# Kernel tuning notes

Hardware: AMD Instinct MI355X
Metric: run time of the kernel (lower is better)

## Reference

```python
import jax, jax.numpy as jnp
import numpy as np

MAX_SEQ_LEN = 1000

def _ln(x, g, b, eps=1e-5):
    m = jnp.mean(x, -1, keepdims=True)
    v = jnp.var(x, -1, keepdims=True)
    return (x - m) * jax.lax.rsqrt(v + eps) * g + b

def _conv1d(x, k, b):
    # x [B,T,Cin], k [K,Cin,Cout], 'SAME' padding (odd kernel)
    return jax.lax.conv_general_dilated(x, k, (1,), 'SAME', dimension_numbers=('NWC', 'WIO', 'NWC')) + b

def _dwconv(x, w):
    # lightweight conv: softmax-normalized depthwise kernel, w [C,K]
    k = jnp.transpose(jax.nn.softmax(w, axis=1))[:, None, :]  # [K,1,C]
    return jax.lax.conv_general_dilated(x, k, (1,), 'SAME', dimension_numbers=('NWC', 'WIO', 'NWC'), feature_group_count=x.shape[-1])

def _conv2d(x, k, b):
    # x [B,H,W,Cin], k [kh,kw,Cin,Cout]
    return jax.lax.conv_general_dilated(x, k, (1, 1), 'SAME', dimension_numbers=('NHWC', 'HWIO', 'NHWC')) + b

def _lconv(x, mask, ln_g, ln_b, glu_w, glu_b, dw, out_w, out_b):
    # LConvBlock: LN -> GLU projection -> depthwise lightweight conv -> out proj -> residual, masked
    res = x
    h = _ln(x, ln_g, ln_b)
    h = h @ glu_w + glu_b
    a, g = jnp.split(h, 2, axis=-1)
    h = a * jax.nn.sigmoid(g)
    h = jnp.where(mask[..., None], 0.0, h)
    h = _dwconv(h, dw)
    h = h @ out_w + out_b
    h = h + res
    return jnp.where(mask[..., None], 0.0, h)

def _forward(content_embedding, speaker_embedding_B, rhythm_B, scaled_duration_outputs,
             in_w, in_b,
             lc0_ln_g, lc0_ln_b, lc0_glu_w, lc0_glu_b, lc0_dw, lc0_out_w, lc0_out_b,
             lc1_ln_g, lc1_ln_b, lc1_glu_w, lc1_glu_b, lc1_dw, lc1_out_w, lc1_out_b,
             p1_w, p1_b, p2_k, p2_b,
             cw_k, cw_b, cw_ln_g, cw_ln_b,
             mkb1_k, mkb1_b, mkb2_k, mkb2_b,
             lw_w, lw_b, ln_g, ln_b, text_mask):
    B, S, _ = content_embedding.shape
    spk = jnp.broadcast_to(speaker_embedding_B[:, None, :], (B, S, speaker_embedding_B.shape[-1]))
    x = jnp.concatenate([content_embedding, spk], -1) @ in_w + in_b
    # duration predictor
    V = _lconv(x, text_mask, lc0_ln_g, lc0_ln_b, lc0_glu_w, lc0_glu_b, lc0_dw, lc0_out_w, lc0_out_b)
    V = _lconv(V, text_mask, lc1_ln_g, lc1_ln_b, lc1_glu_w, lc1_glu_b, lc1_dw, lc1_out_w, lc1_out_b)
    D = jax.nn.softplus(V @ p1_w + p1_b)[..., 0]
    D = jnp.where(text_mask, 0.0, D)
    T = _conv1d(V, p2_k, p2_b)  # [B,S,upsampled_dim]
    # learnable upsampling
    pred_phoneme_len = scaled_duration_outputs.sum(-1)
    alpha_B = jax.lax.stop_gradient(pred_phoneme_len / rhythm_B) / D.sum(-1)
    sD = alpha_B[:, None] * D
    sV = alpha_B[:, None, None] * V
    sT = alpha_B[:, None, None] * T
    mel_len = jnp.clip(jnp.round(sD.sum(-1)).astype(jnp.int32), 1, MAX_SEQ_LEN)
    mel_mask = jnp.arange(MAX_SEQ_LEN)[None, :] >= mel_len[:, None]  # True = pad
    attn_mask = mel_mask[:, :, None] & text_mask[:, None, :]  # bmm(mel_mask, src_mask^T).bool()
    e_k = jnp.cumsum(sD, axis=1)
    s_k = e_k - sD
    t = jnp.arange(1, MAX_SEQ_LEN + 1, dtype=sD.dtype)[None, :, None]
    Sm = jnp.where(attn_mask, 0.0, t - s_k[:, None, :])
    Em = jnp.where(attn_mask, 0.0, e_k[:, None, :] - t)
    # conv_w block: conv1d -> relu -> LN
    Cv = _ln(jax.nn.relu(_conv1d(sV, cw_k, cw_b)), cw_ln_g, cw_ln_b)  # [B,S,CW]
    feat = jnp.concatenate([Sm[..., None], Em[..., None],
                            jnp.broadcast_to(Cv[:, None, :, :], (B, MAX_SEQ_LEN, S, Cv.shape[-1]))], -1)
    h = jax.nn.silu(_conv2d(feat, mkb1_k, mkb1_b))
    h = jax.nn.silu(_conv2d(h, mkb2_k, mkb2_b))
    Wsc = (h @ lw_w + lw_b)[..., 0]  # [B,mel,S]
    Wsc = jnp.where(attn_mask | text_mask[:, None, :], -jnp.inf, Wsc)
    Wmat = jax.nn.softmax(Wsc, axis=2)
    up = jnp.matmul(Wmat, sT)
    up = _ln(up, ln_g, ln_b)
    up = jnp.where(mel_mask[..., None], 0.0, up)
    return up, Wmat, alpha_B, mel_len, mel_mask

def setup_inputs() -> dict:
    key = jax.random.key(0)
    ks = iter(jax.random.split(key, 64))
    B, S, DC, DS, H, CW, MKB, K = 8, 256, 192, 64, 256, 16, 16, 3
    def w(shape, scale=0.02):
        return jax.random.normal(next(ks), shape, jnp.float32) * scale
    inp = {}
    inp['content_embedding'] = jax.random.normal(next(ks), (B, S, DC), jnp.float32)
    inp['speaker_embedding_B'] = jax.random.normal(next(ks), (B, DS), jnp.float32)
    inp['rhythm_B'] = 0.15 + 0.1 * jax.random.uniform(next(ks), (B,), jnp.float32)
    inp['scaled_duration_outputs'] = jax.random.uniform(next(ks), (B, S), jnp.float32)
    lens = jax.random.randint(next(ks), (B,), 200, S + 1)
    inp['text_mask'] = jnp.arange(S)[None, :] >= lens[:, None]
    inp['in_w'] = w((DC + DS, H)); inp['in_b'] = jnp.zeros((H,), jnp.float32)
    for i in range(2):
        inp[f'lc{i}_ln_g'] = jnp.ones((H,), jnp.float32); inp[f'lc{i}_ln_b'] = jnp.zeros((H,), jnp.float32)
        inp[f'lc{i}_glu_w'] = w((H, 2 * H)); inp[f'lc{i}_glu_b'] = jnp.zeros((2 * H,), jnp.float32)
        inp[f'lc{i}_dw'] = w((H, K), 1.0)
        inp[f'lc{i}_out_w'] = w((H, H)); inp[f'lc{i}_out_b'] = jnp.zeros((H,), jnp.float32)
    inp['p1_w'] = w((H, 1)); inp['p1_b'] = jnp.zeros((1,), jnp.float32)
    inp['p2_k'] = w((K, H, H)); inp['p2_b'] = jnp.zeros((H,), jnp.float32)
    inp['cw_k'] = w((K, H, CW)); inp['cw_b'] = jnp.zeros((CW,), jnp.float32)
    inp['cw_ln_g'] = jnp.ones((CW,), jnp.float32); inp['cw_ln_b'] = jnp.zeros((CW,), jnp.float32)
    inp['mkb1_k'] = w((K, K, CW + 2, MKB)); inp['mkb1_b'] = jnp.zeros((MKB,), jnp.float32)
    inp['mkb2_k'] = w((K, K, MKB, MKB)); inp['mkb2_b'] = jnp.zeros((MKB,), jnp.float32)
    inp['lw_w'] = w((MKB, 1)); inp['lw_b'] = jnp.zeros((1,), jnp.float32)
    inp['ln_g'] = jnp.ones((H,), jnp.float32); inp['ln_b'] = jnp.zeros((H,), jnp.float32)
    return inp

def reference(content_embedding, speaker_embedding_B, rhythm_B, scaled_duration_outputs,
              text_mask,
              in_w, in_b,
              lc0_ln_g, lc0_ln_b, lc0_glu_w, lc0_glu_b, lc0_dw, lc0_out_w, lc0_out_b,
              lc1_ln_g, lc1_ln_b, lc1_glu_w, lc1_glu_b, lc1_dw, lc1_out_w, lc1_out_b,
              p1_w, p1_b, p2_k, p2_b,
              cw_k, cw_b, cw_ln_g, cw_ln_b,
              mkb1_k, mkb1_b, mkb2_k, mkb2_b,
              lw_w, lw_b, ln_g, ln_b):
    return _forward(content_embedding, speaker_embedding_B, rhythm_B, scaled_duration_outputs,
                    in_w, in_b,
                    lc0_ln_g, lc0_ln_b, lc0_glu_w, lc0_glu_b, lc0_dw, lc0_out_w, lc0_out_b,
                    lc1_ln_g, lc1_ln_b, lc1_glu_w, lc1_glu_b, lc1_dw, lc1_out_w, lc1_out_b,
                    p1_w, p1_b, p2_k, p2_b,
                    cw_k, cw_b, cw_ln_g, cw_ln_b,
                    mkb1_k, mkb1_b, mkb2_k, mkb2_b,
                    lw_w, lw_b, ln_g, ln_b, text_mask)
```

## Files before the change

kernel.cpp:

```cpp
#include <hip/hip_runtime.h>
#include <math.h>

#define SS 256
#define HH 256
#define MLEN 1000
#define CWW 16
#define NOC 16
#define RB 24

typedef __attribute__((ext_vector_type(8))) short bfrag;
typedef __attribute__((ext_vector_type(4))) float ffrag;

#define WS_V2     1048576u
#define WS_STT    1835008u
#define WS_WB     2097152u
#define WS_CCV    2424832u
#define WS_SSV    2457600u
#define WS_CCI    2490368u
#define WS_SSI    2523136u
#define WS_CP     2555904u
#define WS_CV     2654208u
#define WS_EK     2686976u
#define WS_SK     2689024u
#define WS_ALPHA  2691072u
#define WS_MELI   2691080u
#define WS_TMASK  2691088u

#define PK_IN     0u
#define PK_GLU0   65536u
#define PK_GLU1   196608u
#define PK_OUT0   327680u
#define PK_OUT1   393216u
#define PK_P2     458752u

#define OUT_UP    0u
#define OUT_W     2048000u
#define OUT_ALPHA 4096000u
#define OUT_MLEN  4096008u
#define OUT_MMASK 4096016u

__device__ __forceinline__ unsigned bf16rne(float x){
  unsigned u=__float_as_uint(x);
  u += 0x7fffu + ((u>>16)&1u);
  return u;
}
__device__ __forceinline__ unsigned short bf16h(float x){ return (unsigned short)(bf16rne(x)>>16); }
__device__ __forceinline__ float bf2f(unsigned short u){ return __uint_as_float(((unsigned)u)<<16); }
__device__ __forceinline__ unsigned frag_idx(int k,int n,int KT){
  return (unsigned)(((((n>>4)*KT+(k>>5))*64 + ((k>>3)&3)*16 + (n&15))<<3) + (k&7));
}

__global__ __launch_bounds__(256) void k_prepmask(const void* __restrict__ traw,
    const float* __restrict__ in_w,
    const float* __restrict__ g0, const float* __restrict__ g1,
    const float* __restrict__ o0, const float* __restrict__ o1,
    const float* __restrict__ p2k, float* __restrict__ ws){
  int tid=threadIdx.x;
  if(blockIdx.x==256){
    __shared__ int s_fu, s_ff, s_nz;
    const unsigned char* mb=(const unsigned char*)traw;
    const unsigned int*  mw=(const unsigned int*)traw;
    if(tid==0){s_fu=0;s_ff=0;s_nz=0;}
    __syncthreads();
    int fu=0,ff=0,nz=0;
    for(int w=tid;w<512;w+=256){
      unsigned int v=mw[w];
      if(v){ nz=1; if(v==0x3F800000u) ff=1; else if(v&0xFFFFFF00u) fu=1; }
    }
    if(fu) atomicOr(&s_fu,1);
    if(ff) atomicOr(&s_ff,1);
    if(nz) atomicOr(&s_nz,1);
    __syncthreads();
    int words = (s_ff || (!s_fu && s_nz));
    for(int i=tid;i<2048;i+=256){
      unsigned int v = words ? mw[i] : (unsigned int)mb[i];
      ws[WS_TMASK+i] = v ? 1.0f : 0.0f;
    }
    return;
  }
  unsigned short* wb=(unsigned short*)(ws+WS_WB);
  int gid=blockIdx.x*256+tid, stride=65536;
  for(int i=gid;i<65536;i+=stride){ int k=i>>8,n=i&255; wb[PK_IN  +frag_idx(k,n,8)]=bf16h(in_w[i]); }
  for(int i=gid;i<131072;i+=stride){ int k=i>>9,n=i&511; wb[PK_GLU0+frag_idx(k,n,8)]=bf16h(g0[i]); }
  for(int i=gid;i<131072;i+=stride){ int k=i>>9,n=i&511; wb[PK_GLU1+frag_idx(k,n,8)]=bf16h(g1[i]); }
  for(int i=gid;i<65536;i+=stride){ int k=i>>8,n=i&255; wb[PK_OUT0+frag_idx(k,n,8)]=bf16h(o0[i]); }
  for(int i=gid;i<65536;i+=stride){ int k=i>>8,n=i&255; wb[PK_OUT1+frag_idx(k,n,8)]=bf16h(o1[i]); }
  for(int i=gid;i<196608;i+=stride){ int k3=i>>16,r=i&65535,k=r>>8,n=r&255;
    wb[PK_P2+(unsigned)k3*65536u+frag_idx(k,n,8)]=bf16h(p2k[i]); }
}

__global__ __launch_bounds__(256) void k_front(
    const float* __restrict__ ce, const float* __restrict__ spk,
    const unsigned short* __restrict__ wb, const float* __restrict__ in_b,
    const float* __restrict__ g0b, const float* __restrict__ ln0g, const float* __restrict__ ln0b,
    const float* __restrict__ dw0, const float* __restrict__ o0b,
    const float* __restrict__ g1b, const float* __restrict__ ln1g, const float* __restrict__ ln1b,
    const float* __restrict__ dw1, const float* __restrict__ o1b,
    const float* __restrict__ tmask, float* __restrict__ V2){
  __shared__ unsigned short Abf[16][264];
  __shared__ unsigned short Hb[16][264];
// ... 20 lines not shown
    tmL[tid]=(sI>=0&&sI<256)? tmask[b*256+sI] : 1.0f;
  }
  for(int it=0;it<16;it++){
    float v=0.f;
    int sI=s0-2+it;
    if(it<12 && sI>=0 && sI<256){
      int m=b*256+sI;
      v=(tid<192)? ce[m*192+tid] : spk[b*64+tid-192];
    }
    Abf[it][tid]=bf16h(v);
  }
  __syncthreads();
  {
    ffrag acc[4];
    #pragma unroll
    for(int j=0;j<4;j++){acc[j][0]=0;acc[j][1]=0;acc[j][2]=0;acc[j][3]=0;}
    #pragma unroll
    for(int kt=0;kt<8;kt++){
      bfrag af=*(const bfrag*)&Abf[lm][kt*32+lq*8];
      #pragma unroll
      for(int j=0;j<4;j++){
        int nt=w*4+j;
        bfrag bf=*(const bfrag*)(wb+PK_IN+((((unsigned)(nt*8+kt))*64u+(unsigned)lane)<<3));
        acc[j]=__builtin_amdgcn_mfma_f32_16x16x32_bf16(af,bf,acc[j],0,0,0);
      }
    }
    #pragma unroll
    for(int j=0;j<4;j++){
      int n=w*64+j*16+lm;
      float bn=in_b[n];
      #pragma unroll
      for(int reg=0;reg<4;reg++) Xf[lq*4+reg][n]=acc[j][reg]+bn;
    }
  }
  __syncthreads();
  {
    int r=tid>>4, seg=tid&15;
    if(r<12){
      float s=0.f,q=0.f;
      #pragma unroll
      for(int j4=0;j4<4;j4++){
        float4 v=*(const float4*)&Xf[r][seg*16+j4*4];
        s+=v.x+v.y+v.z+v.w; q+=v.x*v.x+v.y*v.y+v.z*v.z+v.w*v.w;
      }
      s+=__shfl_xor(s,1); q+=__shfl_xor(q,1);
      s+=__shfl_xor(s,2); q+=__shfl_xor(q,2);
      s+=__shfl_xor(s,4); q+=__shfl_xor(q,4);
      s+=__shfl_xor(s,8); q+=__shfl_xor(q,8);
      float mean=s*(1.0f/256.0f), rstd=rsqrtf(q*(1.0f/256.0f)-mean*mean+1e-5f);
      #pragma unroll
      for(int j4=0;j4<4;j4++){
        int c=seg*16+j4*4;
        float4 v=*(const float4*)&Xf[r][c];
        unsigned short q0=bf16h((v.x-mean)*rstd*ln0g[c+0]+ln0b[c+0]);
        unsigned short q1=bf16h((v.y-mean)*rstd*ln0g[c+1]+ln0b[c+1]);
        unsigned short q2=bf16h((v.z-mean)*rstd*ln0g[c+2]+ln0b[c+2]);
        unsigned short q3=bf16h((v.w-mean)*rstd*ln0g[c+3]+ln0b[c+3]);
        *(uint2*)&Abf[r][c]=make_uint2((unsigned)q0|((unsigned)q1<<16),(unsigned)q2|((unsigned)q3<<16));
      }
    } else {
      #pragma unroll
      for(int j4=0;j4<4;j4++) *(uint2*)&Abf[r][seg*16+j4*4]=make_uint2(0,0);
    }
  }
  __syncthreads();
  {
    ffrag aa[4],ag[4];
    #pragma unroll
    for(int j=0;j<4;j++){aa[j][0]=0;aa[j][1]=0;aa[j][2]=0;aa[j][3]=0;
                         ag[j][0]=0;ag[j][1]=0;ag[j][2]=0;ag[j][3]=0;}
    #pragma unroll
    for(int kt=0;kt<8;kt++){
      bfrag af=*(const bfrag*)&Abf[lm][kt*32+lq*8];
      #pragma unroll
      for(int j=0;j<4;j++){
        int nta=w*4+j, ntg=nta+16;
        bfrag bfa=*(const bfrag*)(wb+PK_GLU0+((((unsigned)(nta*8+kt))*64u+(unsigned)lane)<<3));
        bfrag bfg=*(const bfrag*)(wb+PK_GLU0+((((unsigned)(ntg*8+kt))*64u+(unsigned)lane)<<3));
        aa[j]=__builtin_amdgcn_mfma_f32_16x16x32_bf16(af,bfa,aa[j],0,0,0);
        ag[j]=__builtin_amdgcn_mfma_f32_16x16x32_bf16(af,bfg,ag[j],0,0,0);
      }
    }
    __syncthreads();
    #pragma unroll
    for(int j=0;j<4;j++){
      int n=w*64+j*16+lm;
      float ba=g0b[n], bg=g0b[n+256];
      #pragma unroll
      for(int reg=0;reg<4;reg++){
        int row=lq*4+reg;
        float a=aa[j][reg]+ba, g=ag[j][reg]+bg;
        float hv=a*(1.0f/(1.0f+__expf(-g)));
        if(row>=12||tmL[row]!=0.0f) hv=0.0f;
        Hb[row][n]=bf16h(hv);
      }
    }
  }
  __syncthreads();
  {
    float w0=dws[0][0][tid],w1=dws[0][1][tid],w2=dws[0][2][tid];
    for(int r=0;r<10;r++){
      float a=w0*bf2f(Hb[r][tid])+w1*bf2f(Hb[r+1][tid])+w2*bf2f(Hb[r+2][tid]);
      Abf[r][tid]=bf16h(a);
    }
    for(int r=10;r<16;r++) Abf[r][tid]=0;
  }
  __syncthreads();
  {
    ffrag acc[4];
    #pragma unroll
    for(int j=0;j<4;j++){acc[j][0]=0;acc[j][1]=0;acc[j][2]=0;acc[j][3]=0;}
    #pragma unroll
    for(int kt=0;kt<8;kt++){
      bfrag af=*(const bfrag*)&Abf[lm][kt*32+lq*8];
      #pragma unroll
      for(int j=0;j<4;j++){
        int nt=w*4+j;
        bfrag bf=*(const bfrag*)(wb+PK_OUT0+((((unsigned)(nt*8+kt))*64u+(unsigned)lane)<<3));
        acc[j]=__builtin_amdgcn_mfma_f32_16x16x32_bf16(af,bf,acc[j],0,0,0);
      }
    }
    #pragma unroll
    for(int j=0;j<4;j++){
      int n=w*64+j*16+lm;
      float bn=o0b[n];
      #pragma unroll
      for(int reg=0;reg<4;reg++){
        int row=lq*4+reg;
        float v=(row<10 && tmL[row+1]==0.0f)? acc[j][reg]+bn+Xf[row+1][n] : 0.0f;
        Vf[row][n]=v;
      }
    }
  }
  __syncthreads();
  {
    int r=tid>>4, seg=tid&15;
    if(r<10){
      float s=0.f,q=0.f;
      #pragma unroll
      for(int j4=0;j4<4;j4++){
        float4 v=*(const float4*)&Vf[r][seg*16+j4*4];
        s+=v.x+v.y+v.z+v.w; q+=v.x*v.x+v.y*v.y+v.z*v.z+v.w*v.w;
      }
      s+=__shfl_xor(s,1); q+=__shfl_xor(q,1);
      s+=__shfl_xor(s,2); q+=__shfl_xor(q,2);
      s+=__shfl_xor(s,4); q+=__shfl_xor(q,4);
      s+=__shfl_xor(s,8); q+=__shfl_xor(q,8);
      float mean=s*(1.0f/256.0f), rstd=rsqrtf(q*(1.0f/256.0f)-mean*mean+1e-5f);
      #pragma unroll
      for(int j4=0;j4<4;j4++){
        int c=seg*16+j4*4;
        float4 v=*(const float4*)&Vf[r][c];
        unsigned short q0=bf16h((v.x-mean)*rstd*ln1g[c+0]+ln1b[c+0]);
        unsigned short q1=bf16h((v.y-mean)*rstd*ln1g[c+1]+ln1b[c+1]);
        unsigned short q2=bf16h((v.z-mean)*rstd*ln1g[c+2]+ln1b[c+2]);
        unsigned short q3=bf16h((v.w-mean)*rstd*ln1g[c+3]+ln1b[c+3]);
        *(uint2*)&Abf[r][c]=make_uint2((unsigned)q0|((unsigned)q1<<16),(unsigned)q2|((unsigned)q3<<16));
      }
    } else {
      #pragma unroll
      for(int j4=0;j4<4;j4++) *(uint2*)&Abf[r][seg*16+j4*4]=make_uint2(0,0);
    }
  }
  __syncthreads();
  {
    ffrag aa[4],ag[4];
    #pragma unroll
    for(int j=0;j<4;j++){aa[j][0]=0;aa[j][1]=0;aa[j][2]=0;aa[j][3]=0;
                         ag[j][0]=0;ag[j][1]=0;ag[j][2]=0;ag[j][3]=0;}
    #pragma unroll
    for(int kt=0;kt<8;kt++){
      bfrag af=*(const bfrag*)&Abf[lm][kt*32+lq*8];
      #pragma unroll
      for(int j=0;j<4;j++){
        int nta=w*4+j, ntg=nta+16;
        bfrag bfa=*(const bfrag*)(wb+PK_GLU1+((((unsigned)(nta*8+kt))*64u+(unsigned)lane)<<3));
        bfrag bfg=*(const bfrag*)(wb+PK_GLU1+((((unsigned)(ntg*8+kt))*64u+(unsigned)lane)<<3));
        aa[j]=__builtin_amdgcn_mfma_f32_16x16x32_bf16(af,bfa,aa[j],0,0,0);
        ag[j]=__builtin_amdgcn_mfma_f32_16x16x32_bf16(af,bfg,ag[j],0,0,0);
      }
    }
    __syncthreads();
    #pragma unroll
    for(int j=0;j<4;j++){
      int n=w*64+j*16+lm;
      float ba=g1b[n], bg=g1b[n+256];
      #pragma unroll
      for(int reg=0;reg<4;reg++){
        int row=lq*4+reg;
        float a=aa[j][reg]+ba, g=ag[j][reg]+bg;
        float hv=a*(1.0f/(1.0f+__expf(-g)));
        if(row>=10||tmL[row+1]!=0.0f) hv=0.0f;
        Hb[row][n]=bf16h(hv);
      }
    }
  }
  __syncthreads();
  {
    float w0=dws[1][0][tid],w1=dws[1][1][tid],w2=dws[1][2][tid];
    for(int r=0;r<8;r++){
      float a=w0*bf2f(Hb[r][tid])+w1*bf2f(Hb[r+1][tid])+w2*bf2f(Hb[r+2][tid]);
      Abf[r][tid]=bf16h(a);
    }
    for(int r=8;r<16;r++) Abf[r][tid]=0;
  }
  __syncthreads();
  {
    ffrag acc[4];
    #pragma unroll
    for(int j=0;j<4;j++){acc[j][0]=0;acc[j][1]=0;acc[j][2]=0;acc[j][3]=0;}
    #pragma unroll
    for(int kt=0;kt<8;kt++){
      bfrag af=*(const bfrag*)&Abf[lm][kt*32+lq*8];
      #pragma unroll
      for(int j=0;j<4;j++){
        int nt=w*4+j;
        bfrag bf=*(const bfrag*)(wb+PK_OUT1+((((unsigned)(nt*8+kt))*64u+(unsigned)lane)<<3));
        acc[j]=__builtin_amdgcn_mfma_f32_16x16x32_bf16(af,bf,acc[j],0,0,0);
      }
    }
    #pragma unroll
    for(int j=0;j<4;j++){
      int n=w*64+j*16+lm;
      float bn=o1b[n];
      #pragma unroll
      for(int reg=0;reg<4;reg++){
        int row=lq*4+reg;
        if(row<8){
          float v=(tmL[row+2]!=0.0f)? 0.0f : acc[j][reg]+bn+Vf[row+1][n];
          V2[(unsigned)(b*256+s0+row)*256u+n]=v;
        }
      }
    }
  }
}

__global__ __launch_bounds__(256) void k_dur(const float* __restrict__ V2, const float* __restrict__ p1w,
    const float* __restrict__ p1b, const float* __restrict__ sdo, const float* __restrict__ rhythm,
    float* __restrict__ ws, float* __restrict__ outp){
  __shared__ float p1[HH];
  __shared__ float sd[SS];
  __shared__ float red[16];
  int b=blockIdx.x, tid=threadIdx.x;
  int wid=tid>>6, lane=tid&63;
// ... 146 lines not shown
    #pragma unroll
    for(int oc=0;oc<NOC;oc++){ float bb2=mkb1b[oc]; ccv[oc]=bb2; cci[oc]=bb2; ssv[oc]=0.f; ssi[oc]=0.f; }
    for(int dt=0;dt<3;dt++){
      float acc[NOC];
      #pragma unroll
      for(int oc=0;oc<NOC;oc++) acc[oc]=0.f;
      #pragma unroll
      for(int ds=0;ds<3;ds++){
        #pragma unroll
        for(int ic=0;ic<CWW;ic++){
          float v=CvL[tid+ds][ic];
          #pragma unroll
          for(int oc=0;oc<NOC;oc++) acc[oc]+=v*k1c[dt][ds][ic][oc];
        }
      }
      for(int oc=0;oc<NOC;oc++) cpg[(unsigned)(dt*SS+tid)*NOC+oc]=acc[oc];
      float va[16],vb[16],ia[16],ib2[16];
      #pragma unroll
      for(int oc=0;oc<NOC;oc++){ va[oc]=0.f; vb[oc]=0.f; ia[oc]=0.f; ib2[oc]=0.f; }
      #pragma unroll
      for(int ds=0;ds<3;ds++){
        int j=tid+ds;
        float inb=(j>=1&&j<=SS)?1.0f:0.0f;
        float fb=fiE[j];
        float skv=skE[j], ekv=ekE[j];
        #pragma unroll
        for(int oc=0;oc<NOC;oc++){
          float ka=kab[dt][ds][0][oc], kb=kab[dt][ds][1][oc];
          float d=ka-kb, e=kb*ekv-ka*skv;
          va[oc]+=inb*d; vb[oc]+=inb*e; ia[oc]+=fb*d; ib2[oc]+=fb*e;
        }
      }
      float dtf=(float)dt;
      #pragma unroll
      for(int oc=0;oc<NOC;oc++){
        ccv[oc]+=acc[oc]+vb[oc]+dtf*va[oc]; ssv[oc]+=va[oc];
        cci[oc]+=acc[oc]+ib2[oc]+dtf*ia[oc]; ssi[oc]+=ia[oc];
      }
    }
    unsigned base=(unsigned)(b*SS+tid)*16u;
    for(int oc=0;oc<NOC;oc++){
      ws[WS_CCV+base+oc]=ccv[oc];
      ws[WS_SSV+base+oc]=ssv[oc];
      ws[WS_CCI+base+oc]=cci[oc];
      ws[WS_SSI+base+oc]=ssi[oc];
    }
  }
}

__global__ __launch_bounds__(256,4) void k_stageB(
    const float* __restrict__ ws, const float* __restrict__ mkb1k, const float* __restrict__ mkb1b,
    const float* __restrict__ mkb2k, const float* __restrict__ mkb2b,
    const float* __restrict__ lww, const float* __restrict__ lwb,
    float* __restrict__ outp){
  __shared__ short ringh[3][258][RB];
  __shared__ float skL[258], ekL[258];
  __shared__ unsigned char finC[260];
  __shared__ __align__(16) float wscL[SS];
  __shared__ float red[16];
  int bx=blockIdx.x, b=bx/125, chunk=bx%125, t0=chunk*8, tid=threadIdx.x;
  int wid=tid>>6, lane=tid&63;
  int lq=lane>>4, lm=lane&15;
  if(tid<258){
    float sk=0.f, ek=0.f; unsigned char fin=0;
    if(tid>=1 && tid<=SS){
      sk=ws[WS_SK+b*SS+tid-1];
      ek=ws[WS_EK+b*SS+tid-1];
      fin=(ws[WS_TMASK+b*SS+tid-1]!=0.0f)?0:1;
    }
    skL[tid]=sk; ekL[tid]=ek; finC[tid]=fin;
  }
  if(tid<72){
    int sl=tid/24, rem=tid%24;
    int row=(rem<12)?0:257, c=(rem%12)*2;
    *(int*)&ringh[sl][row][c]=0;
  }
  int mel=((const int*)ws)[WS_MELI+b];
  __syncthreads();

  const float* cpb=ws+WS_CP+(unsigned)b*3*SS*NOC;

  unsigned offA[5]; int dtL[5], zgL[5];
  bfrag bfw[5];
  {
    #pragma unroll
    for(int i=0;i<5;i++){
      int g=4*i+lq;
      int dt,ds,hf,zg;
      if(g<18){ dt=g/6; int rm=g-6*dt; ds=rm>>1; hf=rm&1; zg=0; }
      else { dt=0; ds=0; hf=0; zg=1; }
      int srow=wid*64+lm+ds;
      offA[i]=(unsigned)((srow*RB+8*hf)*2);
      dtL[i]=dt; zgL[i]=zg;
      int pk[4];
      if(!zg){
        #pragma unroll
        for(int j=0;j<4;j++){
          unsigned u0=bf16rne(mkb2k[(8*g+2*j)*NOC+lm]);
          unsigned u1=bf16rne(mkb2k[(8*g+2*j+1)*NOC+lm]);
          pk[j]=(int)((u0>>16)|(u1&0xffff0000u));
        }
      } else pk[0]=pk[1]=pk[2]=pk[3]=0;
      bfw[i]=__builtin_bit_cast(bfrag, make_int4(pk[0],pk[1],pk[2],pk[3]));
    }
  }
  float b2v=mkb2b[lm];
  float lwwv=lww[lm];
  float lwb0=lwb[0];
  const char* ringB=(const char*)&ringh[0][0][0];
  bfrag azero={};

  auto conv1row=[&](int T){
    int s=tid;
    float acc[NOC];
    bool fv=(T>=1)&&(T<=998)&&(T+1<mel);
    bool fi=(T>=2)&&(T<=998)&&(T-1>=mel);
    if(fv||fi){
      const float* cc=ws+(fv?WS_CCV:WS_CCI)+(unsigned)(b*SS+s)*16u;
      const float* s2=ws+(fv?WS_SSV:WS_SSI)+(unsigned)(b*SS+s)*16u;
      float Tf=(float)T;
      #pragma unroll
      for(int q=0;q<4;q++){
        float4 c4=((const float4*)cc)[q];
        float4 s4=((const float4*)s2)[q];
        acc[4*q+0]=c4.x+Tf*s4.x; acc[4*q+1]=c4.y+Tf*s4.y;
        acc[4*q+2]=c4.z+Tf*s4.z; acc[4*q+3]=c4.w+Tf*s4.w;
      }
    } else {
      #pragma unroll
      for(int oc=0;oc<NOC;oc++) acc[oc]=mkb1b[oc];
      #pragma unroll
      for(int dt=0;dt<3;dt++){
        int tr=T+dt-1;
        if(tr<0||tr>=MLEN) continue;
        bool valid=(tr<mel);
        float tt=(float)(tr+1);
        float gg[3], hh[3];
        #pragma unroll
        for(int ds=0;ds<3;ds++){
          int j=s+ds;
          float f = valid ? ((j>=1&&j<=SS)?1.0f:0.0f) : (float)finC[j];
          gg[ds]=f*(tt-skL[j]);
          hh[ds]=f*(ekL[j]-tt);
        }
        const float* cpr=cpb+(unsigned)(dt*SS+s)*NOC;
        float4 c0=((const float4*)cpr)[0], c1=((const float4*)cpr)[1];
        float4 c2=((const float4*)cpr)[2], c3=((const float4*)cpr)[3];
        acc[0]+=c0.x; acc[1]+=c0.y; acc[2]+=c0.z; acc[3]+=c0.w;
        acc[4]+=c1.x; acc[5]+=c1.y; acc[6]+=c1.z; acc[7]+=c1.w;
        acc[8]+=c2.x; acc[9]+=c2.y; acc[10]+=c2.z; acc[11]+=c2.w;
        acc[12]+=c3.x; acc[13]+=c3.y; acc[14]+=c3.z; acc[15]+=c3.w;
        #pragma unroll
        for(int ds=0;ds<3;ds++){
          const float* kA=mkb1k+((dt*3+ds)*18+0)*NOC;
          const float* kB=mkb1k+((dt*3+ds)*18+1)*NOC;
          #pragma unroll
          for(int oc=0;oc<NOC;oc++) acc[oc]+=gg[ds]*kA[oc]+hh[ds]*kB[oc];
        }
      }
    }
    int slot=T%3;
    int pk[8];
    #pragma unroll
    for(int j=0;j<8;j++){
      float x0=acc[2*j], x1=acc[2*j+1];
      float s0=x0/(1.0f+__expf(-x0));
      float s1=x1/(1.0f+__expf(-x1));
      unsigned u0=bf16rne(s0), u1=bf16rne(s1);
      pk[j]=(int)((u0>>16)|(u1&0xffff0000u));
    }
    int4* dst=(int4*)&ringh[slot][s+1][0];
    dst[0]=make_int4(pk[0],pk[1],pk[2],pk[3]);
    dst[1]=make_int4(pk[4],pk[5],pk[6],pk[7]);
  };

  if(t0>0) conv1row(t0-1);
  conv1row(t0);

  #pragma unroll 1
  for(int r=0;r<8;r++){
    int t=t0+r;
    if(t+1<MLEN) conv1row(t+1);
    __syncthreads();
    int tmod=t%3;
    ffrag acc2[4];
    #pragma unroll
    for(int tt=0;tt<4;tt++){ acc2[tt][0]=b2v; acc2[tt][1]=b2v; acc2[tt][2]=b2v; acc2[tt][3]=b2v; }
    #pragma unroll
    for(int i=0;i<5;i++){
      int dt=dtL[i];
      int x=tmod+dt+2; x=(x>=3)?x-3:x; x=(x>=3)?x-3:x;
      int tr=t+dt-1;
      bool av=((unsigned)tr<(unsigned)MLEN)&&(!zgL[i]);
      const char* rp=ringB+(unsigned)x*(258u*RB*2u)+offA[i];
      #pragma unroll
      for(int tt=0;tt<4;tt++){
        int4 ra=*(const int4*)(rp+tt*(16*RB*2));
        bfrag a=av?__builtin_bit_cast(bfrag,ra):azero;
        acc2[tt]=__builtin_amdgcn_mfma_f32_16x16x32_bf16(a,bfw[i],acc2[tt],0,0,0);
      }
    }
    #pragma unroll
    for(int tt=0;tt<4;tt++){
      float out4[4];
      #pragma unroll
      for(int q=0;q<4;q++){
        float xx=acc2[tt][q];
        float pv=(xx/(1.0f+__expf(-xx)))*lwwv;
        pv+=__shfl_xor(pv,1); pv+=__shfl_xor(pv,2); pv+=__shfl_xor(pv,4); pv+=__shfl_xor(pv,8);
        out4[q]=pv+lwb0;
      }
      if(lm==0){
        *(float4*)&wscL[wid*64+tt*16+lq*4]=make_float4(out4[0],out4[1],out4[2],out4[3]);
      }
    }
    __syncthreads();
    float fm=(float)finC[tid+1];
    float wsc=wscL[tid];
    float val=(fm!=0.0f)?wsc:-3.0e38f;
    float mx=val;
    for(int off=32;off;off>>=1) mx=fmaxf(mx,__shfl_down(mx,off));
    if(lane==0) red[wid]=mx;
    __syncthreads();
    mx=fmaxf(fmaxf(red[0],red[1]),fmaxf(red[2],red[3]));
    float e=(fm!=0.0f)?__expf(wsc-mx):0.0f;
    float sm=e;
    for(int off=32;off;off>>=1) sm+=__shfl_down(sm,off);
    if(lane==0) red[8+wid]=sm;
    __syncthreads();
    sm=red[8]+red[9]+red[10]+red[11];
    outp[OUT_W+(unsigned)(b*MLEN+t)*SS+tid]=e/sm;
    __syncthreads();
  }
}

__global__ __launch_bounds__(256) void k_up(const float* __restrict__ ws,
    const float* __restrict__ lng, const float* __restrict__ lnb, float* __restrict__ outp){
  __shared__ unsigned short Wbf[16][264];
  __shared__ float UpL[16][264];
  __shared__ float gb[2][256];
  int bx=blockIdx.x, b=bx/63, tile=bx%63, t0=tile*16, tid=threadIdx.x;
  gb[0][tid]=lng[tid]; gb[1][tid]=lnb[tid];
  for(int it=0;it<16;it++){
    int t=t0+it;
    float v=(t<MLEN)? outp[OUT_W+(unsigned)(b*MLEN+t)*256u+tid] : 0.0f;
    Wbf[it][tid]=bf16h(v);
  }
  int mel=((const int*)ws)[WS_MELI+b];
  __syncthreads();
  int w=tid>>6, lane=tid&63, lq=lane>>4, lm=lane&15;
  const unsigned short* stt=(const unsigned short*)(ws+WS_STT)+(unsigned)b*65536u;
  ffrag acc[4];
  #pragma unroll
  for(int tt=0;tt<4;tt++){ acc[tt][0]=0;acc[tt][1]=0;acc[tt][2]=0;acc[tt][3]=0; }
  #pragma unroll
  for(int kt=0;kt<8;kt++){
    bfrag af=*(const bfrag*)&Wbf[lm][kt*32+lq*8];
    #pragma unroll
    for(int tt=0;tt<4;tt++){
      int n=w*64+tt*16+lm;
      bfrag bf=*(const bfrag*)(stt+((unsigned)n<<8)+(unsigned)(kt*32+lq*8));
      acc[tt]=__builtin_amdgcn_mfma_f32_16x16x32_bf16(af,bf,acc[tt],0,0,0);
    }
  }
  #pragma unroll
  for(int tt=0;tt<4;tt++){
    #pragma unroll
    for(int reg=0;reg<4;reg++)
      UpL[lq*4+reg][w*64+tt*16+lm]=acc[tt][reg];
  }
  __syncthreads();
  int r=tid>>4, seg=tid&15;
  float s=0.f,q=0.f;
  #pragma unroll
  for(int j4=0;j4<4;j4++){
    float4 v=*(const float4*)&UpL[r][seg*16+j4*4];
    s+=v.x+v.y+v.z+v.w; q+=v.x*v.x+v.y*v.y+v.z*v.z+v.w*v.w;
  }
  s+=__shfl_xor(s,1); q+=__shfl_xor(q,1);
  s+=__shfl_xor(s,2); q+=__shfl_xor(q,2);
  s+=__shfl_xor(s,4); q+=__shfl_xor(q,4);
  s+=__shfl_xor(s,8); q+=__shfl_xor(q,8);
  float mean=s*(1.0f/256.0f), rstd=rsqrtf(q*(1.0f/256.0f)-mean*mean+1e-5f);
  int t=t0+r;
  if(t<MLEN){
    bool vld=(t<mel);
    #pragma unroll
    for(int j4=0;j4<4;j4++){
      int c=seg*16+j4*4;
      float4 v=*(const float4*)&UpL[r][c];
      float4 o;
      o.x=vld?((v.x-mean)*rstd*gb[0][c+0]+gb[1][c+0]):0.0f;
      o.y=vld?((v.y-mean)*rstd*gb[0][c+1]+gb[1][c+1]):0.0f;
      o.z=vld?((v.z-mean)*rstd*gb[0][c+2]+gb[1][c+2]):0.0f;
      o.w=vld?((v.w-mean)*rstd*gb[0][c+3]+gb[1][c+3]):0.0f;
      *(float4*)&outp[OUT_UP+(unsigned)(b*MLEN+t)*256u+c]=o;
    }
  }
}

extern "C" void kernel_launch(void* const* d_in, const int* in_sizes, int n_in,
                              void* d_out, int out_size, void* d_ws, size_t ws_size,
                              hipStream_t stream){
  const float* ce   =(const float*)d_in[0];
  const float* spk  =(const float*)d_in[1];
  const float* rhy  =(const float*)d_in[2];
  const float* sdo  =(const float*)d_in[3];
  const void*  tmr  =d_in[4];
  const float* in_w =(const float*)d_in[5];
  const float* in_b =(const float*)d_in[6];
  const float* l0lg =(const float*)d_in[7];
  const float* l0lb =(const float*)d_in[8];
  const float* l0gw =(const float*)d_in[9];
  const float* l0gb =(const float*)d_in[10];
  const float* l0dw =(const float*)d_in[11];
  const float* l0ow =(const float*)d_in[12];
  const float* l0ob =(const float*)d_in[13];
  const float* l1lg =(const float*)d_in[14];
  const float* l1lb =(const float*)d_in[15];
  const float* l1gw =(const float*)d_in[16];
  const float* l1gb =(const float*)d_in[17];
  const float* l1dw =(const float*)d_in[18];
  const float* l1ow =(const float*)d_in[19];
  const float* l1ob =(const float*)d_in[20];
  const float* p1w  =(const float*)d_in[21];
  const float* p1b  =(const float*)d_in[22];
  const float* p2k  =(const float*)d_in[23];
  const float* p2b  =(const float*)d_in[24];
  const float* cwk  =(const float*)d_in[25];
  const float* cwb  =(const float*)d_in[26];
  const float* cwg  =(const float*)d_in[27];
  const float* cwbe =(const float*)d_in[28];
  const float* m1k  =(const float*)d_in[29];
  const float* m1b  =(const float*)d_in[30];
  const float* m2k  =(const float*)d_in[31];
  const float* m2b  =(const float*)d_in[32];
  const float* lww  =(const float*)d_in[33];
  const float* lwbp =(const float*)d_in[34];
  const float* lng  =(const float*)d_in[35];
  const float* lnb  =(const float*)d_in[36];
  float* ws=(float*)d_ws;
  float* outp=(float*)d_out;
  const unsigned short* wbb=(const unsigned short*)(ws+WS_WB);

  k_prepmask<<<257,256,0,stream>>>(tmr, in_w, l0gw, l1gw, l0ow, l1ow, p2k, ws);
  k_front   <<<256,256,0,stream>>>(ce, spk, wbb, in_b,
                                   l0gb, l0lg, l0lb, l0dw, l0ob,
                                   l1gb, l1lg, l1lb, l1dw, l1ob,
                                   ws+WS_TMASK, ws+WS_V2);
  k_dur     <<<8,256,0,stream>>>(ws+WS_V2, p1w, p1b, sdo, rhy, ws, outp);
  k_post    <<<392,256,0,stream>>>(ws+WS_V2, wbb+PK_P2, p2b, cwk, cwb, cwg, cwbe, m1k, m1b, ws);
  k_stageB  <<<1000,256,0,stream>>>(ws, m1k, m1b, m2k, m2b, lww, lwbp, outp);
  k_up      <<<504,256,0,stream>>>(ws, lng, lnb, outp);
}
```

Measured before the change: 313.2 us.

## Fuse upsample LayerNorm kernel into stageB and swap MFMA operand roles

Removes the separate k_up kernel. Each stageB block now computes the W@STT upsample matmul and LayerNorm for its own 8 frames, reusing the ring LDS buffer. This drops one launch and the separate pass that reread the attention weights. The second conv's MFMA operands are swapped so each lane holds four output channels, which replaces the 16-lane shuffle reduction with a few xor-shuffles. Out-of-range rows are now zero-filled in the ring, so the per-fragment validity selects go away. In exchange, half of each 16-row MFMA tile is wasted on zero padding, since blocks only cover 8 frames.

```diff
diff --git a/kernel.cpp b/kernel.cpp
--- a/kernel.cpp
+++ b/kernel.cpp
@@ -562,8 +562,9 @@
     const float* __restrict__ ws, const float* __restrict__ mkb1k, const float* __restrict__ mkb1b,
     const float* __restrict__ mkb2k, const float* __restrict__ mkb2b,
     const float* __restrict__ lww, const float* __restrict__ lwb,
+    const float* __restrict__ lng, const float* __restrict__ lnb,
     float* __restrict__ outp){
-  __shared__ short ringh[3][258][RB];
+  __shared__ __align__(16) short ringh[3][258][RB];
   __shared__ float skL[258], ekL[258];
   __shared__ unsigned char finC[260];
   __shared__ __align__(16) float wscL[SS];
@@ -590,20 +591,20 @@
 
   const float* cpb=ws+WS_CP+(unsigned)b*3*SS*NOC;
 
-  unsigned offA[5]; int dtL[5], zgL[5];
+  unsigned offA[5]; int dtL[5];
   bfrag bfw[5];
   {
     #pragma unroll
     for(int i=0;i<5;i++){
       int g=4*i+lq;
-      int dt,ds,hf,zg;
-      if(g<18){ dt=g/6; int rm=g-6*dt; ds=rm>>1; hf=rm&1; zg=0; }
-      else { dt=0; ds=0; hf=0; zg=1; }
+      int dt,ds,hf;
+      if(g<18){ dt=g/6; int rm=g-6*dt; ds=rm>>1; hf=rm&1; }
+      else { dt=0; ds=0; hf=0; }
       int srow=wid*64+lm+ds;
       offA[i]=(unsigned)((srow*RB+8*hf)*2);
-      dtL[i]=dt; zgL[i]=zg;
+      dtL[i]=dt;
       int pk[4];
-      if(!zg){
+      if(g<18){
         #pragma unroll
         for(int j=0;j<4;j++){
           unsigned u0=bf16rne(mkb2k[(8*g+2*j)*NOC+lm]);
@@ -614,13 +615,19 @@
       bfw[i]=__builtin_bit_cast(bfrag, make_int4(pk[0],pk[1],pk[2],pk[3]));
     }
   }
-  float b2v=mkb2b[lm];
-  float lwwv=lww[lm];
+  float4 b2q=*(const float4*)&mkb2b[lq*4];
+  float4 lw4=*(const float4*)&lww[lq*4];
   float lwb0=lwb[0];
   const char* ringB=(const char*)&ringh[0][0][0];
-  bfrag azero={};
 
   auto conv1row=[&](int T){
+    int slot=((T%3)+3)%3;
+    int4* dst=(int4*)&ringh[slot][tid+1][0];
+    if((unsigned)T>=(unsigned)MLEN){
+      dst[0]=make_int4(0,0,0,0);
+      dst[1]=make_int4(0,0,0,0);
+      return;
+    }
     int s=tid;
     float acc[NOC];
     bool fv=(T>=1)&&(T<=998)&&(T+1<mel);
@@ -669,7 +676,6 @@
         }
       }
     }
-    int slot=T%3;
     int pk[8];
     #pragma unroll
     for(int j=0;j<8;j++){
@@ -679,50 +685,43 @@
       unsigned u0=bf16rne(s0), u1=bf16rne(s1);
       pk[j]=(int)((u0>>16)|(u1&0xffff0000u));
     }
-    int4* dst=(int4*)&ringh[slot][s+1][0];
     dst[0]=make_int4(pk[0],pk[1],pk[2],pk[3]);
     dst[1]=make_int4(pk[4],pk[5],pk[6],pk[7]);
   };
 
-  if(t0>0) conv1row(t0-1);
+  conv1row(t0-1);
   conv1row(t0);
 
   #pragma unroll 1
   for(int r=0;r<8;r++){
     int t=t0+r;
-    if(t+1<MLEN) conv1row(t+1);
+    conv1row(t+1);
     __syncthreads();
     int tmod=t%3;
     ffrag acc2[4];
     #pragma unroll
-    for(int tt=0;tt<4;tt++){ acc2[tt][0]=b2v; acc2[tt][1]=b2v; acc2[tt][2]=b2v; acc2[tt][3]=b2v; }
+    for(int tt=0;tt<4;tt++){ acc2[tt][0]=b2q.x; acc2[tt][1]=b2q.y; acc2[tt][2]=b2q.z; acc2[tt][3]=b2q.w; }
     #pragma unroll
     for(int i=0;i<5;i++){
       int dt=dtL[i];
       int x=tmod+dt+2; x=(x>=3)?x-3:x; x=(x>=3)?x-3:x;
-      int tr=t+dt-1;
-      bool av=((unsigned)tr<(unsigned)MLEN)&&(!zgL[i]);
       const char* rp=ringB+(unsigned)x*(258u*RB*2u)+offA[i];
       #pragma unroll
       for(int tt=0;tt<4;tt++){
-        int4 ra=*(const int4*)(rp+tt*(16*RB*2));
-        bfrag a=av?__builtin_bit_cast(bfrag,ra):azero;
-        acc2[tt]=__builtin_amdgcn_mfma_f32_16x16x32_bf16(a,bfw[i],acc2[tt],0,0,0);
+        bfrag a=*(const bfrag*)(rp+tt*(16*RB*2));
+        acc2[tt]=__builtin_amdgcn_mfma_f32_16x16x32_bf16(bfw[i],a,acc2[tt],0,0,0);
       }
     }
     #pragma unroll
     for(int tt=0;tt<4;tt++){
-      float out4[4];
-      #pragma unroll
-      for(int q=0;q<4;q++){
-        float xx=acc2[tt][q];
-        float pv=(xx/(1.0f+__expf(-xx)))*lwwv;
-        pv+=__shfl_xor(pv,1); pv+=__shfl_xor(pv,2); pv+=__shfl_xor(pv,4); pv+=__shfl_xor(pv,8);
-        out4[q]=pv+lwb0;
-      }
-      if(lm==0){
-        *(float4*)&wscL[wid*64+tt*16+lq*4]=make_float4(out4[0],out4[1],out4[2],out4[3]);
-      }
+      float x0=acc2[tt][0], x1=acc2[tt][1], x2=acc2[tt][2], x3=acc2[tt][3];
+      float pvs=(x0/(1.0f+__expf(-x0)))*lw4.x
+               +(x1/(1.0f+__expf(-x1)))*lw4.y
+               +(x2/(1.0f+__expf(-x2)))*lw4.z
+               +(x3/(1.0f+__expf(-x3)))*lw4.w;
+      pvs+=__shfl_xor(pvs,16);
+      pvs+=__shfl_xor(pvs,32);
+      if(lane<16) wscL[wid*64+tt*16+lane]=pvs+lwb0;
     }
     __syncthreads();
     float fm=(float)finC[tid+1];
@@ -739,72 +738,71 @@
     if(lane==0) red[8+wid]=sm;
     __syncthreads();
     sm=red[8]+red[9]+red[10]+red[11];
-    outp[OUT_W+(unsigned)(b*MLEN+t)*SS+tid]=e/sm;
-    __syncthreads();
-  }
-}
-
-__global__ __launch_bounds__(256) void k_up(const float* __restrict__ ws,
-    const float* __restrict__ lng, const float* __restrict__ lnb, float* __restrict__ outp){
-  __shared__ unsigned short Wbf[16][264];
-  __shared__ float UpL[16][264];
-  __shared__ float gb[2][256];
-  int bx=blockIdx.x, b=bx/63, tile=bx%63, t0=tile*16, tid=threadIdx.x;
-  gb[0][tid]=lng[tid]; gb[1][tid]=lnb[tid];
-  for(int it=0;it<16;it++){
-    int t=t0+it;
-    float v=(t<MLEN)? outp[OUT_W+(unsigned)(b*MLEN+t)*256u+tid] : 0.0f;
-    Wbf[it][tid]=bf16h(v);
-  }
-  int mel=((const int*)ws)[WS_MELI+b];
-  __syncthreads();
-  int w=tid>>6, lane=tid&63, lq=lane>>4, lm=lane&15;
+    float p=e*(1.0f/sm);
+    outp[OUT_W+(unsigned)(b*MLEN+t)*SS+tid]=p;
+    __syncthreads();
+  }
+
+  unsigned short (*Wbf)[264]=(unsigned short(*)[264])&ringh[0][0][0];
+  float (*UpL)[264]=(float(*)[264])((char*)&ringh[0][0][0]+8448);
+  skL[tid]=lng[tid];
+  ekL[tid]=lnb[tid];
+  #pragma unroll
+  for(int rr=0;rr<8;rr++){
+    Wbf[rr][tid]=bf16h(outp[OUT_W+(unsigned)(b*MLEN+t0+rr)*SS+tid]);
+    Wbf[rr+8][tid]=0;
+  }
+  __syncthreads();
   const unsigned short* stt=(const unsigned short*)(ws+WS_STT)+(unsigned)b*65536u;
-  ffrag acc[4];
-  #pragma unroll
-  for(int tt=0;tt<4;tt++){ acc[tt][0]=0;acc[tt][1]=0;acc[tt][2]=0;acc[tt][3]=0; }
-  #pragma unroll
-  for(int kt=0;kt<8;kt++){
-    bfrag af=*(const bfrag*)&Wbf[lm][kt*32+lq*8];
+  {
+    ffrag acc[4];
+    #pragma unroll
+    for(int tt=0;tt<4;tt++){ acc[tt][0]=0;acc[tt][1]=0;acc[tt][2]=0;acc[tt][3]=0; }
+    #pragma unroll
+    for(int kt=0;kt<8;kt++){
+      bfrag af=*(const bfrag*)&Wbf[lm][kt*32+lq*8];
+      #pragma unroll
+      for(int tt=0;tt<4;tt++){
+        int n=wid*64+tt*16+lm;
+        bfrag bf=*(const bfrag*)(stt+((unsigned)n<<8)+(unsigned)(kt*32+lq*8));
+        acc[tt]=__builtin_amdgcn_mfma_f32_16x16x32_bf16(af,bf,acc[tt],0,0,0);
+      }
+    }
     #pragma unroll
     for(int tt=0;tt<4;tt++){
-      int n=w*64+tt*16+lm;
-      bfrag bf=*(const bfrag*)(stt+((unsigned)n<<8)+(unsigned)(kt*32+lq*8));
-      acc[tt]=__builtin_amdgcn_mfma_f32_16x16x32_bf16(af,bf,acc[tt],0,0,0);
-    }
-  }
-  #pragma unroll
-  for(int tt=0;tt<4;tt++){
-    #pragma unroll
-    for(int reg=0;reg<4;reg++)
-      UpL[lq*4+reg][w*64+tt*16+lm]=acc[tt][reg];
-  }
-  __syncthreads();
-  int r=tid>>4, seg=tid&15;
-  float s=0.f,q=0.f;
-  #pragma unroll
-  for(int j4=0;j4<4;j4++){
-    float4 v=*(const float4*)&UpL[r][seg*16+j4*4];
-    s+=v.x+v.y+v.z+v.w; q+=v.x*v.x+v.y*v.y+v.z*v.z+v.w*v.w;
-  }
-  s+=__shfl_xor(s,1); q+=__shfl_xor(q,1);
-  s+=__shfl_xor(s,2); q+=__shfl_xor(q,2);
-  s+=__shfl_xor(s,4); q+=__shfl_xor(q,4);
-  s+=__shfl_xor(s,8); q+=__shfl_xor(q,8);
-  float mean=s*(1.0f/256.0f), rstd=rsqrtf(q*(1.0f/256.0f)-mean*mean+1e-5f);
-  int t=t0+r;
-  if(t<MLEN){
-    bool vld=(t<mel);
+      #pragma unroll
+      for(int reg=0;reg<4;reg++)
+        UpL[lq*4+reg][wid*64+tt*16+lm]=acc[tt][reg];
+    }
+  }
+  __syncthreads();
+  {
+    int r=tid>>4, seg=tid&15;
+    float s=0.f,q=0.f;
     #pragma unroll
     for(int j4=0;j4<4;j4++){
-      int c=seg*16+j4*4;
-      float4 v=*(const float4*)&UpL[r][c];
-      float4 o;
-      o.x=vld?((v.x-mean)*rstd*gb[0][c+0]+gb[1][c+0]):0.0f;
-      o.y=vld?((v.y-mean)*rstd*gb[0][c+1]+gb[1][c+1]):0.0f;
-      o.z=vld?((v.z-mean)*rstd*gb[0][c+2]+gb[1][c+2]):0.0f;
-      o.w=vld?((v.w-mean)*rstd*gb[0][c+3]+gb[1][c+3]):0.0f;
-      *(float4*)&outp[OUT_UP+(unsigned)(b*MLEN+t)*256u+c]=o;
+      float4 v=*(const float4*)&UpL[r][seg*16+j4*4];
+      s+=v.x+v.y+v.z+v.w; q+=v.x*v.x+v.y*v.y+v.z*v.z+v.w*v.w;
+    }
+    s+=__shfl_xor(s,1); q+=__shfl_xor(q,1);
+    s+=__shfl_xor(s,2); q+=__shfl_xor(q,2);
+    s+=__shfl_xor(s,4); q+=__shfl_xor(q,4);
+    s+=__shfl_xor(s,8); q+=__shfl_xor(q,8);
+    float mean=s*(1.0f/256.0f), rstd=rsqrtf(q*(1.0f/256.0f)-mean*mean+1e-5f);
+    if(r<8){
+      int t=t0+r;
+      bool vld=(t<mel);
+      #pragma unroll
+      for(int j4=0;j4<4;j4++){
+        int c=seg*16+j4*4;
+        float4 v=*(const float4*)&UpL[r][c];
+        float4 o;
+        o.x=vld?((v.x-mean)*rstd*skL[c+0]+ekL[c+0]):0.0f;
+        o.y=vld?((v.y-mean)*rstd*skL[c+1]+ekL[c+1]):0.0f;
+        o.z=vld?((v.z-mean)*rstd*skL[c+2]+ekL[c+2]):0.0f;
+        o.w=vld?((v.w-mean)*rstd*skL[c+3]+ekL[c+3]):0.0f;
+        *(float4*)&outp[OUT_UP+(unsigned)(b*MLEN+t)*256u+c]=o;
+      }
     }
   }
 }
@@ -860,6 +858,5 @@
                                    ws+WS_TMASK, ws+WS_V2);
   k_dur     <<<8,256,0,stream>>>(ws+WS_V2, p1w, p1b, sdo, rhy, ws, outp);
   k_post    <<<392,256,0,stream>>>(ws+WS_V2, wbb+PK_P2, p2b, cwk, cwb, cwg, cwbe, m1k, m1b, ws);
-  k_stageB  <<<1000,256,0,stream>>>(ws, m1k, m1b, m2k, m2b, lww, lwbp, outp);
-  k_up      <<<504,256,0,stream>>>(ws, lng, lnb, outp);
+  k_stageB  <<<1000,256,0,stream>>>(ws, m1k, m1b, m2k, m2b, lww, lwbp, lng, lnb, outp);
 }
```

Result: no change. 315.5 us (+0.7%).

## Add closed-form conv1 fast path, drop softmax max pass, pack bf16 conversions

Applied to the files above, without the earlier changes.

Adds a fast path for interior tiles that fully lie inside or outside the mel length. There the first conv row is computed as an affine function of T from precomputed per-channel coefficients instead of the full convolution. The softmax over 256 columns skips the max-subtraction pass, uses transposed MFMA operands so the lw reduction needs only two shuffles, and moves the next row's conv1 after the barrier to cut syncs. It also uses v_cvt_pk_bf16_f32 and rcp for sigmoid and bf16 packing. Skipping the max may overflow exp if the logits are large, and the fast path relies on precomputed WS_CCV/WS_SSV tables being correct.

```diff
diff --git a/kernel.cpp b/kernel.cpp
--- a/kernel.cpp
+++ b/kernel.cpp
@@ -46,6 +46,14 @@
 }
 __device__ __forceinline__ unsigned short bf16h(float x){ return (unsigned short)(bf16rne(x)>>16); }
 __device__ __forceinline__ float bf2f(unsigned short u){ return __uint_as_float(((unsigned)u)<<16); }
+__device__ __forceinline__ int cvtpk(float lo, float hi){
+  int r;
+  asm("v_cvt_pk_bf16_f32 %0, %1, %2" : "=v"(r) : "v"(lo), "v"(hi));
+  return r;
+}
+__device__ __forceinline__ float fsig(float x){
+  return __builtin_amdgcn_rcpf(1.0f+__expf(-x));
+}
 __device__ __forceinline__ unsigned frag_idx(int k,int n,int KT){
   return (unsigned)(((((n>>4)*KT+(k>>5))*64 + ((k>>3)&3)*16 + (n&15))<<3) + (k&7));
 }
@@ -172,11 +180,9 @@
       for(int j4=0;j4<4;j4++){
         int c=seg*16+j4*4;
         float4 v=*(const float4*)&Xf[r][c];
-        unsigned short q0=bf16h((v.x-mean)*rstd*ln0g[c+0]+ln0b[c+0]);
-        unsigned short q1=bf16h((v.y-mean)*rstd*ln0g[c+1]+ln0b[c+1]);
-        unsigned short q2=bf16h((v.z-mean)*rstd*ln0g[c+2]+ln0b[c+2]);
-        unsigned short q3=bf16h((v.w-mean)*rstd*ln0g[c+3]+ln0b[c+3]);
-        *(uint2*)&Abf[r][c]=make_uint2((unsigned)q0|((unsigned)q1<<16),(unsigned)q2|((unsigned)q3<<16));
+        int p0=cvtpk((v.x-mean)*rstd*ln0g[c+0]+ln0b[c+0],(v.y-mean)*rstd*ln0g[c+1]+ln0b[c+1]);
+        int p1=cvtpk((v.z-mean)*rstd*ln0g[c+2]+ln0b[c+2],(v.w-mean)*rstd*ln0g[c+3]+ln0b[c+3]);
+        *(uint2*)&Abf[r][c]=make_uint2((unsigned)p0,(unsigned)p1);
       }
     } else {
       #pragma unroll
@@ -210,7 +216,7 @@
       for(int reg=0;reg<4;reg++){
         int row=lq*4+reg;
         float a=aa[j][reg]+ba, g=ag[j][reg]+bg;
-        float hv=a*(1.0f/(1.0f+__expf(-g)));
+        float hv=a*fsig(g);
         if(row>=12||tmL[row]!=0.0f) hv=0.0f;
         Hb[row][n]=bf16h(hv);
       }
@@ -271,11 +277,9 @@
       for(int j4=0;j4<4;j4++){
         int c=seg*16+j4*4;
         float4 v=*(const float4*)&Vf[r][c];
-        unsigned short q0=bf16h((v.x-mean)*rstd*ln1g[c+0]+ln1b[c+0]);
-        unsigned short q1=bf16h((v.y-mean)*rstd*ln1g[c+1]+ln1b[c+1]);
-        unsigned short q2=bf16h((v.z-mean)*rstd*ln1g[c+2]+ln1b[c+2]);
-        unsigned short q3=bf16h((v.w-mean)*rstd*ln1g[c+3]+ln1b[c+3]);
-        *(uint2*)&Abf[r][c]=make_uint2((unsigned)q0|((unsigned)q1<<16),(unsigned)q2|((unsigned)q3<<16));
+        int p0=cvtpk((v.x-mean)*rstd*ln1g[c+0]+ln1b[c+0],(v.y-mean)*rstd*ln1g[c+1]+ln1b[c+1]);
+        int p1=cvtpk((v.z-mean)*rstd*ln1g[c+2]+ln1b[c+2],(v.w-mean)*rstd*ln1g[c+3]+ln1b[c+3]);
+        *(uint2*)&Abf[r][c]=make_uint2((unsigned)p0,(unsigned)p1);
       }
     } else {
       #pragma unroll
@@ -309,7 +313,7 @@
       for(int reg=0;reg<4;reg++){
         int row=lq*4+reg;
         float a=aa[j][reg]+ba, g=ag[j][reg]+bg;
-        float hv=a*(1.0f/(1.0f+__expf(-g)));
+        float hv=a*fsig(g);
         if(row>=10||tmL[row+1]!=0.0f) hv=0.0f;
         Hb[row][n]=bf16h(hv);
       }
@@ -563,7 +567,7 @@
     const float* __restrict__ mkb2k, const float* __restrict__ mkb2b,
     const float* __restrict__ lww, const float* __restrict__ lwb,
     float* __restrict__ outp){
-  __shared__ short ringh[3][258][RB];
+  __shared__ __align__(16) short ringh[3][258][RB];
   __shared__ float skL[258], ekL[258];
   __shared__ unsigned char finC[260];
   __shared__ __align__(16) float wscL[SS];
@@ -590,20 +594,20 @@
 
   const float* cpb=ws+WS_CP+(unsigned)b*3*SS*NOC;
 
-  unsigned offA[5]; int dtL[5], zgL[5];
+  unsigned offA[5]; int dtL[5];
   bfrag bfw[5];
   {
     #pragma unroll
     for(int i=0;i<5;i++){
       int g=4*i+lq;
-      int dt,ds,hf,zg;
-      if(g<18){ dt=g/6; int rm=g-6*dt; ds=rm>>1; hf=rm&1; zg=0; }
-      else { dt=0; ds=0; hf=0; zg=1; }
+      int dt,ds,hf;
+      if(g<18){ dt=g/6; int rm=g-6*dt; ds=rm>>1; hf=rm&1; }
+      else { dt=0; ds=0; hf=0; }
       int srow=wid*64+lm+ds;
       offA[i]=(unsigned)((srow*RB+8*hf)*2);
-      dtL[i]=dt; zgL[i]=zg;
+      dtL[i]=dt;
       int pk[4];
-      if(!zg){
+      if(g<18){
         #pragma unroll
         for(int j=0;j<4;j++){
           unsigned u0=bf16rne(mkb2k[(8*g+2*j)*NOC+lm]);
@@ -614,13 +618,50 @@
       bfw[i]=__builtin_bit_cast(bfrag, make_int4(pk[0],pk[1],pk[2],pk[3]));
     }
   }
-  float b2v=mkb2b[lm];
-  float lwwv=lww[lm];
+  float4 b2q=*(const float4*)&mkb2b[lq*4];
+  float4 lw4=*(const float4*)&lww[lq*4];
   float lwb0=lwb[0];
   const char* ringB=(const char*)&ringh[0][0][0];
-  bfrag azero={};
-
-  auto conv1row=[&](int T){
+
+  bool pureV=(t0>=2)&&(t0<=990)&&(t0+9<mel);
+  bool pureI=(t0>=3)&&(t0<=990)&&(t0-2>=mel);
+  bool pure=pureV||pureI;
+  float ccR[16], ssR[16];
+  if(pure){
+    const float* cc=ws+(pureV?WS_CCV:WS_CCI)+(unsigned)(b*SS+tid)*16u;
+    const float* s2=ws+(pureV?WS_SSV:WS_SSI)+(unsigned)(b*SS+tid)*16u;
+    #pragma unroll
+    for(int q=0;q<4;q++){
+      float4 c4=((const float4*)cc)[q];
+      float4 s4=((const float4*)s2)[q];
+      ccR[4*q+0]=c4.x; ccR[4*q+1]=c4.y; ccR[4*q+2]=c4.z; ccR[4*q+3]=c4.w;
+      ssR[4*q+0]=s4.x; ssR[4*q+1]=s4.y; ssR[4*q+2]=s4.z; ssR[4*q+3]=s4.w;
+    }
+  }
+
+  auto conv1fast=[&](int T){
+    int slot=T%3;
+    float Tf=(float)T;
+    int pk[8];
+    #pragma unroll
+    for(int j=0;j<8;j++){
+      float x0=fmaf(Tf,ssR[2*j+0],ccR[2*j+0]);
+      float x1=fmaf(Tf,ssR[2*j+1],ccR[2*j+1]);
+      pk[j]=cvtpk(x0*fsig(x0),x1*fsig(x1));
+    }
+    int4* dst=(int4*)&ringh[slot][tid+1][0];
+    dst[0]=make_int4(pk[0],pk[1],pk[2],pk[3]);
+    dst[1]=make_int4(pk[4],pk[5],pk[6],pk[7]);
+  };
+
+  auto conv1gen=[&](int T){
+    int slot=((T%3)+3)%3;
+    int4* dst=(int4*)&ringh[slot][tid+1][0];
+    if((unsigned)T>=(unsigned)MLEN){
+      dst[0]=make_int4(0,0,0,0);
+      dst[1]=make_int4(0,0,0,0);
+      return;
+    }
     int s=tid;
     float acc[NOC];
     bool fv=(T>=1)&&(T<=998)&&(T+1<mel);
@@ -669,78 +710,63 @@
         }
       }
     }
-    int slot=T%3;
     int pk[8];
     #pragma unroll
     for(int j=0;j<8;j++){
       float x0=acc[2*j], x1=acc[2*j+1];
-      float s0=x0/(1.0f+__expf(-x0));
-      float s1=x1/(1.0f+__expf(-x1));
-      unsigned u0=bf16rne(s0), u1=bf16rne(s1);
-      pk[j]=(int)((u0>>16)|(u1&0xffff0000u));
-    }
-    int4* dst=(int4*)&ringh[slot][s+1][0];
+      pk[j]=cvtpk(x0*fsig(x0),x1*fsig(x1));
+    }
     dst[0]=make_int4(pk[0],pk[1],pk[2],pk[3]);
     dst[1]=make_int4(pk[4],pk[5],pk[6],pk[7]);
   };
 
-  if(t0>0) conv1row(t0-1);
-  conv1row(t0);
+  if(pure){ conv1fast(t0-1); conv1fast(t0); conv1fast(t0+1); }
+  else    { conv1gen (t0-1); conv1gen (t0); conv1gen (t0+1); }
+  __syncthreads();
 
   #pragma unroll 1
   for(int r=0;r<8;r++){
     int t=t0+r;
-    if(t+1<MLEN) conv1row(t+1);
-    __syncthreads();
     int tmod=t%3;
     ffrag acc2[4];
     #pragma unroll
-    for(int tt=0;tt<4;tt++){ acc2[tt][0]=b2v; acc2[tt][1]=b2v; acc2[tt][2]=b2v; acc2[tt][3]=b2v; }
+    for(int tt=0;tt<4;tt++){ acc2[tt][0]=b2q.x; acc2[tt][1]=b2q.y; acc2[tt][2]=b2q.z; acc2[tt][3]=b2q.w; }
     #pragma unroll
     for(int i=0;i<5;i++){
       int dt=dtL[i];
       int x=tmod+dt+2; x=(x>=3)?x-3:x; x=(x>=3)?x-3:x;
-      int tr=t+dt-1;
-      bool av=((unsigned)tr<(unsigned)MLEN)&&(!zgL[i]);
       const char* rp=ringB+(unsigned)x*(258u*RB*2u)+offA[i];
       #pragma unroll
       for(int tt=0;tt<4;tt++){
-        int4 ra=*(const int4*)(rp+tt*(16*RB*2));
-        bfrag a=av?__builtin_bit_cast(bfrag,ra):azero;
-        acc2[tt]=__builtin_amdgcn_mfma_f32_16x16x32_bf16(a,bfw[i],acc2[tt],0,0,0);
-      }
-    }
+        bfrag a=*(const bfrag*)(rp+tt*(16*RB*2));
+        acc2[tt]=__builtin_amdgcn_mfma_f32_16x16x32_bf16(bfw[i],a,acc2[tt],0,0,0);
+      }
+    }
+    float esum=0.f;
     #pragma unroll
     for(int tt=0;tt<4;tt++){
-      float out4[4];
-      #pragma unroll
-      for(int q=0;q<4;q++){
-        float xx=acc2[tt][q];
-        float pv=(xx/(1.0f+__expf(-xx)))*lwwv;
-        pv+=__shfl_xor(pv,1); pv+=__shfl_xor(pv,2); pv+=__shfl_xor(pv,4); pv+=__shfl_xor(pv,8);
-        out4[q]=pv+lwb0;
-      }
-      if(lm==0){
-        *(float4*)&wscL[wid*64+tt*16+lq*4]=make_float4(out4[0],out4[1],out4[2],out4[3]);
-      }
-    }
-    __syncthreads();
-    float fm=(float)finC[tid+1];
-    float wsc=wscL[tid];
-    float val=(fm!=0.0f)?wsc:-3.0e38f;
-    float mx=val;
-    for(int off=32;off;off>>=1) mx=fmaxf(mx,__shfl_down(mx,off));
-    if(lane==0) red[wid]=mx;
-    __syncthreads();
-    mx=fmaxf(fmaxf(red[0],red[1]),fmaxf(red[2],red[3]));
-    float e=(fm!=0.0f)?__expf(wsc-mx):0.0f;
-    float sm=e;
-    for(int off=32;off;off>>=1) sm+=__shfl_down(sm,off);
-    if(lane==0) red[8+wid]=sm;
-    __syncthreads();
-    sm=red[8]+red[9]+red[10]+red[11];
-    outp[OUT_W+(unsigned)(b*MLEN+t)*SS+tid]=e/sm;
-    __syncthreads();
+      float pvs=acc2[tt][0]*fsig(acc2[tt][0])*lw4.x
+               +acc2[tt][1]*fsig(acc2[tt][1])*lw4.y
+               +acc2[tt][2]*fsig(acc2[tt][2])*lw4.z
+               +acc2[tt][3]*fsig(acc2[tt][3])*lw4.w;
+      pvs+=__shfl_xor(pvs,16);
+      pvs+=__shfl_xor(pvs,32);
+      int s=wid*64+tt*16+lm;
+      float fm=(float)finC[1+s];
+      float ev=fm*__expf(pvs+lwb0);
+      if(lane<16) wscL[s]=ev;
+      esum+=ev;
+    }
+    esum+=__shfl_xor(esum,1);
+    esum+=__shfl_xor(esum,2);
+    esum+=__shfl_xor(esum,4);
+    esum+=__shfl_xor(esum,8);
+    if(lane==0) red[wid]=esum;
+    __syncthreads();
+    if(r<7){ if(pure) conv1fast(t+2); else conv1gen(t+2); }
+    float tot=red[0]+red[1]+red[2]+red[3];
+    outp[OUT_W+(unsigned)(b*MLEN+t)*SS+tid]=wscL[tid]*__builtin_amdgcn_rcpf(tot);
+    if(r<7) __syncthreads();
   }
 }
 
```

New measurement: 287.7 us. -8.1%, faster.
